# Kernel tuning notes

Measured on AMD Instinct MI355X. Metric: run time of the kernel, lower is better.

## Reference

```python
import jax, jax.numpy as jnp
import numpy as np

N, F, D, H, E = 100000, 256, 128, 4, 1000000
C = D // H  # out_channels per head


def setup_inputs() -> dict:
    key = jax.random.key(0)
    ks = jax.random.split(key, 10)
    glorot = lambda k, shp, fan: jax.random.normal(k, shp, jnp.float32) * (2.0 / sum(fan)) ** 0.5
    return {
        "x": jax.random.normal(ks[0], (N, F), jnp.float32),
        "edge_index_0": jax.random.randint(ks[1], (2, E), 0, N, jnp.int32),
        "edge_index_1": jax.random.randint(ks[2], (2, E), 0, N, jnp.int32),
        "W_lin": glorot(ks[3], (F, D), (F, D)),
        "b_lin": jnp.zeros((D,), jnp.float32),
        "attn_l": glorot(ks[4], (2, H, C), (H, C)),
        "attn_r": glorot(ks[5], (2, H, C), (H, C)),
        "alpha_act": jnp.ones((2,), jnp.float32),  # 'sharpening' init 1.0
        "W_conv": glorot(ks[6], (3, F), (F, 3)),
        "b_conv": jnp.zeros((3,), jnp.float32),
    }


def _segment_softmax(a, seg, n):
    # a: [E, H], seg: [E] destination indices
    amax = jax.ops.segment_max(a, seg, num_segments=n)  # [N, H], -inf for empty segs
    ex = jnp.exp(a - amax[seg])
    denom = jax.ops.segment_sum(ex, seg, num_segments=n)
    return ex / denom[seg]


def reference(x, edge_index_0, edge_index_1, W_lin, b_lin, attn_l, attn_r, alpha_act, W_conv, b_conv):
    # get_h_dict: Linear(F -> D) then reshape [N, H, C]
    h = x @ W_lin + b_lin                      # [N, D]
    hh = h.reshape(N, H, C)
    # get_beta_weights: Conv1d(F, 3, kernel_size=1) on x.unsqueeze(-1) == linear per node; softmax over relations
    beta = jax.nn.softmax(x @ W_conv.T + b_conv, axis=1)  # [N, 3]

    # agg_relation_neighbors: per-metapath GAT-style attention + scatter-add
    rel_outs = []
    for m, ei in enumerate((edge_index_0, edge_index_1)):
        al = jnp.sum(hh * attn_l[m], axis=-1)  # [N, H]
        ar = jnp.sum(hh * attn_r[m], axis=-1)  # [N, H]
        dst, src_j = ei[0], ei[1]              # flow target_to_source: aggregate at edge_index[0]
        a = (ar[src_j] + al[dst]) * alpha_act[m]   # message alpha_j + alpha_i, sharpening activation
        alpha = _segment_softmax(a, dst, N)        # softmax per destination node
        msg = hh[src_j] * alpha[:, :, None]        # [E, H, C]
        rel_outs.append(jax.ops.segment_sum(msg, dst, num_segments=N).reshape(N, D))
    # last relation slot holds the node's own h (first=True)
    emb = jnp.stack(rel_outs + [h], axis=1)        # [N, 3, D]
    out = jnp.einsum('nrd,nr->nd', emb, beta)      # matmul(emb^T, beta).squeeze(-1)
    return jax.nn.relu(out)                        # embedding_activation 'relu'
```

## Files before the change

kernel.cpp:

```cpp
#include <hip/hip_runtime.h>
#include <hip/hip_bf16.h>

#define NN 100000
#define FF 256
#define DD 128
#define EE 1000000
#define NPX (NN / 8)
#define PART_BLOCKS 1024
#define PART_CHUNK ((2 * EE) / (PART_BLOCKS / 8))

typedef __attribute__((ext_vector_type(4))) float f32x4;
typedef __attribute__((ext_vector_type(8))) short bf16x8;

__device__ __forceinline__ ushort f2bf(float f) {
    __hip_bfloat16 h = __float2bfloat16(f);
    return *reinterpret_cast<ushort*>(&h);
}
__device__ __forceinline__ float bf2f(ushort u) {
    return __uint_as_float(((uint)u) << 16);
}

__global__ void pack_w(const float* __restrict__ Wl, ushort* __restrict__ Wt) {
    int id = blockIdx.x * 256 + threadIdx.x;
    int k = id >> 7, n = id & 127;
    Wt[n * FF + k] = f2bf(Wl[id]);
}

__global__ __launch_bounds__(256) void fused_h(const float* __restrict__ x,
                                               const ushort* __restrict__ Wt,
                                               const float* __restrict__ bl,
                                               const float* __restrict__ Wc,
                                               const float* __restrict__ bc,
                                               ushort* __restrict__ hb,
                                               float* __restrict__ beta) {
    __shared__ ushort xs[64][72];
    __shared__ ushort wsT[128][72];
    __shared__ ushort hs[64][136];
    __shared__ float wcs[768];

    int t = threadIdx.x;
    int wv = t >> 6, lane = t & 63;
    int row0 = blockIdx.x * 64;
    int br = t >> 2, bq = t & 3;
    bool rowok = (row0 + br) < NN;

    if (t < 192) ((float4*)wcs)[t] = ((const float4*)Wc)[t];
    __syncthreads();

    f32x4 acc[8];
    #pragma unroll
    for (int i = 0; i < 8; ++i) acc[i] = (f32x4){0.f, 0.f, 0.f, 0.f};

    float bs0 = 0.f, bs1 = 0.f, bs2 = 0.f;

    for (int k0 = 0; k0 < FF; k0 += 64) {
        if (rowok) {
            const float4* xp = (const float4*)(x + (size_t)(row0 + br) * FF + k0 + bq * 16);
            #pragma unroll
            for (int j = 0; j < 4; ++j) {
                float4 v = xp[j];
                int kk = bq * 16 + j * 4;
                const float* w0 = wcs + k0 + kk;
                bs0 += v.x * w0[0] + v.y * w0[1] + v.z * w0[2] + v.w * w0[3];
                const float* w1 = wcs + 256 + k0 + kk;
                bs1 += v.x * w1[0] + v.y * w1[1] + v.z * w1[2] + v.w * w1[3];
                const float* w2 = wcs + 512 + k0 + kk;
                bs2 += v.x * w2[0] + v.y * w2[1] + v.z * w2[2] + v.w * w2[3];
                ushort4 p;
                p.x = f2bf(v.x); p.y = f2bf(v.y); p.z = f2bf(v.z); p.w = f2bf(v.w);
                *(ushort4*)&xs[br][kk] = p;
            }
        } else {
            ushort4 z = {0, 0, 0, 0};
            #pragma unroll
            for (int j = 0; j < 4; ++j) *(ushort4*)&xs[br][bq * 16 + j * 4] = z;
        }
        #pragma unroll
        for (int j = 0; j < 4; ++j) {
            int c = t + 256 * j;
            int rw = c >> 3, seg = c & 7;
            uint4 v = *(const uint4*)(Wt + rw * FF + k0 + seg * 8);
            *(uint4*)&wsT[rw][seg * 8] = v;
        }
        __syncthreads();
        #pragma unroll
        for (int ks = 0; ks < 2; ++ks) {
            bf16x8 af = *(const bf16x8*)&xs[wv * 16 + (lane & 15)][ks * 32 + (lane >> 4) * 8];
            #pragma unroll
            for (int nt = 0; nt < 8; ++nt) {
                bf16x8 bv = *(const bf16x8*)&wsT[nt * 16 + (lane & 15)][ks * 32 + (lane >> 4) * 8];
                acc[nt] = __builtin_amdgcn_mfma_f32_16x16x32_bf16(af, bv, acc[nt], 0, 0, 0);
            }
        }
        __syncthreads();
    }

    bs0 += __shfl_xor(bs0, 1); bs0 += __shfl_xor(bs0, 2);
    bs1 += __shfl_xor(bs1, 1); bs1 += __shfl_xor(bs1, 2);
    bs2 += __shfl_xor(bs2, 1); bs2 += __shfl_xor(bs2, 2);
    if (bq == 0 && rowok) {
        float s0 = bs0 + bc[0], s1 = bs1 + bc[1], s2 = bs2 + bc[2];
        float mx = fmaxf(s0, fmaxf(s1, s2));
        float e0 = __expf(s0 - mx), e1 = __expf(s1 - mx), e2 = __expf(s2 - mx);
        float inv = 1.f / (e0 + e1 + e2);
        int n = row0 + br;
        beta[n * 3 + 0] = e0 * inv;
        beta[n * 3 + 1] = e1 * inv;
        beta[n * 3 + 2] = e2 * inv;
    }

    #pragma unroll
    for (int nt = 0; nt < 8; ++nt) {
        int col = nt * 16 + (lane & 15);
        float bias = bl[col];
        int rbase = wv * 16 + (lane >> 4) * 4;
        #pragma unroll
        for (int r = 0; r < 4; ++r) {
            hs[rbase + r][col] = f2bf(acc[nt][r] + bias);
        }
    }
    __syncthreads();
    #pragma unroll
    for (int j = 0; j < 4; ++j) {
        int c = t + 256 * j;
        int rw = c >> 4, seg = c & 15;
        if (row0 + rw < NN) {
            uint4 v = *(const uint4*)&hs[rw][seg * 8];
            *(uint4*)(hb + (size_t)(row0 + rw) * DD + seg * 8) = v;
        }
    }
}

__global__ __launch_bounds__(256) void alr_kernel(const ushort* __restrict__ hb,
                                                  const float* __restrict__ attn_l,
                                                  const float* __restrict__ attn_r,
                                                  float* __restrict__ AL,
                                                  float* __restrict__ AR) {
    int wid = threadIdx.x >> 6, lane = threadIdx.x & 63;
    int n = blockIdx.x * 4 + wid;
    uint hv = ((const uint*)hb)[(size_t)n * 64 + lane];
    float hx = bf2f((ushort)(hv & 0xffff)), hy = bf2f((ushort)(hv >> 16));
    int hd = lane >> 4;
    int cg = lane & 15;
    #pragma unroll
    for (int m = 0; m < 2; ++m) {
        float2 wl = ((const float2*)attn_l)[m * 64 + hd * 16 + cg];
        float2 wr = ((const float2*)attn_r)[m * 64 + hd * 16 + cg];
        float sl = hx * wl.x + hy * wl.y;
        float sr = hx * wr.x + hy * wr.y;
        for (int off = 1; off < 16; off <<= 1) {
            sl += __shfl_xor(sl, off);
            sr += __shfl_xor(sr, off);
        }
        if (cg == 0) {
            AL[(size_t)(m * NN + n) * 4 + hd] = sl;
            AR[(size_t)(m * NN + n) * 4 + hd] = sr;
        }
    }
}

__global__ __launch_bounds__(256) void count_kernel(const int* __restrict__ ei0,
                                                    const int* __restrict__ ei1,
                                                    int* __restrict__ deg) {
    int b = blockIdx.x;
    int lo = (b & 7) * NPX, hi = lo + NPX;
    int e0 = (b >> 3) * PART_CHUNK;
    for (int i = threadIdx.x; i < PART_CHUNK; i += 256) {
        int e = e0 + i;
        int dst, base;
        if (e < EE) { dst = ei0[e]; base = 0; }
        else        { dst = ei1[e - EE]; base = NN; }
        if (dst >= lo && dst < hi) atomicAdd(&deg[base + dst], 1);
    }
}

__global__ __launch_bounds__(256) void scatter_kernel(const int* __restrict__ ei0,
                                                      const int* __restrict__ ei1,
                                                      const int* __restrict__ rp,
                                                      int* __restrict__ cursor,
                                                      int* __restrict__ srcs) {
    int b = blockIdx.x;
    int lo = (b & 7) * NPX, hi = lo + NPX;
    int e0 = (b >> 3) * PART_CHUNK;
    for (int i = threadIdx.x; i < PART_CHUNK; i += 256) {
        int e = e0 + i;
        int dst, src, base;
        if (e < EE) { dst = ei0[e]; src = ei0[EE + e]; base = 0; }
        else        { int ee = e - EE; dst = ei1[ee]; src = ei1[EE + ee]; base = NN; }
        if (dst >= lo && dst < hi) {
            int idx = base + dst;
            int pos = rp[idx] + atomicAdd(&cursor[idx], 1);
            srcs[pos] = src;
        }
    }
}

__global__ __launch_bounds__(256) void scan1(const int* __restrict__ deg, int* __restrict__ rp,
                                             int* __restrict__ bsum, int L) {
    __shared__ int sm[256];
    int t = threadIdx.x;
    int i = blockIdx.x * 256 + t;
    int v = (i < L) ? deg[i] : 0;
    sm[t] = v;
    __syncthreads();
    for (int off = 1; off < 256; off <<= 1) {
        int o = (t >= off) ? sm[t - off] : 0;
        __syncthreads();
        sm[t] += o;
        __syncthreads();
    }
    if (i < L) rp[i] = sm[t] - v;
    if (t == 255) bsum[blockIdx.x] = sm[255];
}

__global__ __launch_bounds__(256) void scan2(int* __restrict__ bsum, int nb) {
    __shared__ int sm[256];
    int t = threadIdx.x;
    int carry = 0;
    for (int base = 0; base < nb; base += 256) {
        int i = base + t;
        int v = (i < nb) ? bsum[i] : 0;
        __syncthreads();
        sm[t] = v;
        __syncthreads();
        for (int off = 1; off < 256; off <<= 1) {
            int o = (t >= off) ? sm[t - off] : 0;
            __syncthreads();
            sm[t] += o;
            __syncthreads();
        }
        int incl = sm[t];
        int tot = sm[255];
        if (i < nb) bsum[i] = carry + incl - v;
        carry += tot;
    }
}

__global__ void scan3(int* __restrict__ rp, const int* __restrict__ bsum, int L) {
    int i = blockIdx.x * 256 + threadIdx.x;
    if (i < L) rp[i] += bsum[blockIdx.x];
    if (i == 0) rp[L] = 2 * EE;
}

__global__ __launch_bounds__(256) void main_kernel(const ushort* __restrict__ hb,
                                                   const float* __restrict__ AL,
                                                   const float* __restrict__ AR,
                                                   const float* __restrict__ beta,
                                                   const float* __restrict__ alpha_act,
                                                   const int* __restrict__ rp,
                                                   const int* __restrict__ srcs,
                                                   float* __restrict__ out) {
    __shared__ float2 contribs[2][64];
    int w = threadIdx.x >> 6, lane = threadIdx.x & 63;
    int slot = w >> 1, m = w & 1;
    int n = blockIdx.x * 2 + slot;
    const uint* h2 = (const uint*)hb;
    int hd = lane >> 4;

    float alv = AL[(size_t)(m * NN + n) * 4 + hd];
    float am = alpha_act[m];
    float bm = beta[n * 3 + m];
    int e0 = rp[m * NN + n];
    int e1 = rp[m * NN + n + 1];
    const float* ARm = AR + (size_t)m * NN * 4;

    float denom = 0.f, ax = 0.f, ay = 0.f;
    for (int e = e0; e < e1; e += 4) {
        int last = e1 - 1;
        int i1 = min(e + 1, last), i2 = min(e + 2, last), i3 = min(e + 3, last);
        int s0 = srcs[e], s1 = srcs[i1], s2 = srcs[i2], s3 = srcs[i3];
        float r0 = ARm[s0 * 4 + hd];
        float r1 = ARm[s1 * 4 + hd];
        float r2 = ARm[s2 * 4 + hd];
        float r3 = ARm[s3 * 4 + hd];
        uint g0 = h2[(size_t)s0 * 64 + lane];
        uint g1 = h2[(size_t)s1 * 64 + lane];
        uint g2 = h2[(size_t)s2 * 64 + lane];
        uint g3 = h2[(size_t)s3 * 64 + lane];
        float v1 = (e + 1 < e1) ? 1.f : 0.f;
        float v2 = (e + 2 < e1) ? 1.f : 0.f;
        float v3 = (e + 3 < e1) ? 1.f : 0.f;
        float p0 = __expf((r0 + alv) * am);
        float p1 = v1 * __expf((r1 + alv) * am);
        float p2 = v2 * __expf((r2 + alv) * am);
        float p3 = v3 * __expf((r3 + alv) * am);
        denom += (p0 + p1) + (p2 + p3);
        ax += p0 * bf2f((ushort)(g0 & 0xffff)) + p1 * bf2f((ushort)(g1 & 0xffff))
            + p2 * bf2f((ushort)(g2 & 0xffff)) + p3 * bf2f((ushort)(g3 & 0xffff));
        ay += p0 * bf2f((ushort)(g0 >> 16)) + p1 * bf2f((ushort)(g1 >> 16))
            + p2 * bf2f((ushort)(g2 >> 16)) + p3 * bf2f((ushort)(g3 >> 16));
    }
    float invd = (denom > 0.f) ? (1.f / denom) : 0.f;
    float cx = bm * ax * invd;
    float cy = bm * ay * invd;

    if (m == 1) contribs[slot][lane] = make_float2(cx, cy);
    __syncthreads();
    if (m == 0) {
        uint hv = h2[(size_t)n * 64 + lane];
        float b2 = beta[n * 3 + 2];
        float2 c1 = contribs[slot][lane];
        float ox = b2 * bf2f((ushort)(hv & 0xffff)) + cx + c1.x;
        float oy = b2 * bf2f((ushort)(hv >> 16)) + cy + c1.y;
        float2 res;
        res.x = fmaxf(ox, 0.f);
        res.y = fmaxf(oy, 0.f);
        ((float2*)out)[(size_t)n * 64 + lane] = res;
    }
}

extern "C" void kernel_launch(void* const* d_in, const int* in_sizes, int n_in,
                              void* d_out, int out_size, void* d_ws, size_t ws_size,
                              hipStream_t stream) {
    const float* x      = (const float*)d_in[0];
    const int*   ei0    = (const int*)d_in[1];
    const int*   ei1    = (const int*)d_in[2];
    const float* W_lin  = (const float*)d_in[3];
    const float* b_lin  = (const float*)d_in[4];
    const float* attn_l = (const float*)d_in[5];
    const float* attn_r = (const float*)d_in[6];
    const float* alpha  = (const float*)d_in[7];
    const float* W_conv = (const float*)d_in[8];
    const float* b_conv = (const float*)d_in[9];
    float* out = (float*)d_out;

    char* ws = (char*)d_ws;
    size_t off = 0;
    ushort* hb   = (ushort*)(ws + off); off += (size_t)NN * DD * 2;
    ushort* Wt   = (ushort*)(ws + off); off += (size_t)DD * FF * 2;
    float* AL    = (float*)(ws + off);  off += (size_t)2 * NN * 4 * 4;
    float* AR    = (float*)(ws + off);  off += (size_t)2 * NN * 4 * 4;
    float* beta  = (float*)(ws + off);  off += (size_t)NN * 3 * 4;
    int*   deg   = (int*)(ws + off);    off += (size_t)2 * NN * 4;
    int*   cursor= (int*)(ws + off);    off += (size_t)2 * NN * 4;
    int*   rp    = (int*)(ws + off);    off += ((size_t)2 * NN + 4) * 4;
    int*   bsum  = (int*)(ws + off);    off += 1024 * 4;
    int*   srcs  = (int*)(ws + off);    off += (size_t)2 * EE * 4;

    hipMemsetAsync(deg, 0, (size_t)4 * NN * 4, stream);

    pack_w<<<DD * FF / 256, 256, 0, stream>>>(W_lin, Wt);
    fused_h<<<(NN + 63) / 64, 256, 0, stream>>>(x, Wt, b_lin, W_conv, b_conv, hb, beta);
    alr_kernel<<<NN / 4, 256, 0, stream>>>(hb, attn_l, attn_r, AL, AR);
    count_kernel<<<PART_BLOCKS, 256, 0, stream>>>(ei0, ei1, deg);
    int L = 2 * NN;
    int nb = (L + 255) / 256;
    scan1<<<nb, 256, 0, stream>>>(deg, rp, bsum, L);
    scan2<<<1, 256, 0, stream>>>(bsum, nb);
    scan3<<<nb, 256, 0, stream>>>(rp, bsum, L);
    scatter_kernel<<<PART_BLOCKS, 256, 0, stream>>>(ei0, ei1, rp, cursor, srcs);
    main_kernel<<<NN / 2, 256, 0, stream>>>(hb, AL, AR, beta, alpha, rp, srcs, out);
}
```

Baseline: 354.8 us.

## Vectorize edge partition loads and split wave into two edge halves in main kernel

The count and scatter kernels now split work per relation into fixed 8192-edge chunks and read the edge index with int4 loads, with more blocks launched. The main kernel has each half-wave handle alternate edges, with each lane loading 4 bf16 features (uint2) and using 32-bit offset arithmetic. The two halves' partial sums are combined with shuffles, aiming for more gathers in flight per node. The remainder check (e+4<=EE) holds because EE is divisible by 4, and half the lanes sit idle in the epilogue.

```diff
diff --git a/kernel.cpp b/kernel.cpp
--- a/kernel.cpp
+++ b/kernel.cpp
@@ -6,8 +6,8 @@
 #define DD 128
 #define EE 1000000
 #define NPX (NN / 8)
-#define PART_BLOCKS 1024
-#define PART_CHUNK ((2 * EE) / (PART_BLOCKS / 8))
+#define CH 8192
+#define NCH 123
 
 typedef __attribute__((ext_vector_type(4))) float f32x4;
 typedef __attribute__((ext_vector_type(8))) short bf16x8;
@@ -164,13 +164,20 @@
                                                     int* __restrict__ deg) {
     int b = blockIdx.x;
     int lo = (b & 7) * NPX, hi = lo + NPX;
-    int e0 = (b >> 3) * PART_CHUNK;
-    for (int i = threadIdx.x; i < PART_CHUNK; i += 256) {
-        int e = e0 + i;
-        int dst, base;
-        if (e < EE) { dst = ei0[e]; base = 0; }
-        else        { dst = ei1[e - EE]; base = NN; }
-        if (dst >= lo && dst < hi) atomicAdd(&deg[base + dst], 1);
+    int q = b >> 3;
+    int rel = q / NCH, ch = q - rel * NCH;
+    const int* dstrow = rel ? ei1 : ei0;
+    int base = rel * NN;
+    int e0 = ch * CH;
+    for (int i = threadIdx.x; i < CH / 4; i += 256) {
+        int e = e0 + i * 4;
+        if (e + 4 <= EE) {
+            int4 d = *(const int4*)(dstrow + e);
+            if (d.x >= lo && d.x < hi) atomicAdd(&deg[base + d.x], 1);
+            if (d.y >= lo && d.y < hi) atomicAdd(&deg[base + d.y], 1);
+            if (d.z >= lo && d.z < hi) atomicAdd(&deg[base + d.z], 1);
+            if (d.w >= lo && d.w < hi) atomicAdd(&deg[base + d.w], 1);
+        }
     }
 }
 
@@ -181,16 +188,20 @@
                                                       int* __restrict__ srcs) {
     int b = blockIdx.x;
     int lo = (b & 7) * NPX, hi = lo + NPX;
-    int e0 = (b >> 3) * PART_CHUNK;
-    for (int i = threadIdx.x; i < PART_CHUNK; i += 256) {
-        int e = e0 + i;
-        int dst, src, base;
-        if (e < EE) { dst = ei0[e]; src = ei0[EE + e]; base = 0; }
-        else        { int ee = e - EE; dst = ei1[ee]; src = ei1[EE + ee]; base = NN; }
-        if (dst >= lo && dst < hi) {
-            int idx = base + dst;
-            int pos = rp[idx] + atomicAdd(&cursor[idx], 1);
-            srcs[pos] = src;
+    int q = b >> 3;
+    int rel = q / NCH, ch = q - rel * NCH;
+    const int* row = rel ? ei1 : ei0;
+    int base = rel * NN;
+    int e0 = ch * CH;
+    for (int i = threadIdx.x; i < CH / 4; i += 256) {
+        int e = e0 + i * 4;
+        if (e + 4 <= EE) {
+            int4 d = *(const int4*)(row + e);
+            int4 s = *(const int4*)(row + EE + e);
+            if (d.x >= lo && d.x < hi) { int idx = base + d.x; srcs[rp[idx] + atomicAdd(&cursor[idx], 1)] = s.x; }
+            if (d.y >= lo && d.y < hi) { int idx = base + d.y; srcs[rp[idx] + atomicAdd(&cursor[idx], 1)] = s.y; }
+            if (d.z >= lo && d.z < hi) { int idx = base + d.z; srcs[rp[idx] + atomicAdd(&cursor[idx], 1)] = s.z; }
+            if (d.w >= lo && d.w < hi) { int idx = base + d.w; srcs[rp[idx] + atomicAdd(&cursor[idx], 1)] = s.w; }
         }
     }
 }
@@ -250,62 +261,57 @@
                                                    const int* __restrict__ rp,
                                                    const int* __restrict__ srcs,
                                                    float* __restrict__ out) {
-    __shared__ float2 contribs[2][64];
+    __shared__ float4 contribs[2][32];
     int w = threadIdx.x >> 6, lane = threadIdx.x & 63;
     int slot = w >> 1, m = w & 1;
     int n = blockIdx.x * 2 + slot;
-    const uint* h2 = (const uint*)hb;
-    int hd = lane >> 4;
+    int half = lane >> 5, sl = lane & 31;
+    int hd = sl >> 3;
+    const char* h8 = (const char*)hb;
+    const char* ar8 = (const char*)(AR + (size_t)m * NN * 4);
+    const char* sr8 = (const char*)srcs;
+    uint aoff = (uint)(hd << 2);
+    uint hoff = (uint)(sl << 3);
 
     float alv = AL[(size_t)(m * NN + n) * 4 + hd];
     float am = alpha_act[m];
-    float bm = beta[n * 3 + m];
     int e0 = rp[m * NN + n];
     int e1 = rp[m * NN + n + 1];
-    const float* ARm = AR + (size_t)m * NN * 4;
-
-    float denom = 0.f, ax = 0.f, ay = 0.f;
-    for (int e = e0; e < e1; e += 4) {
-        int last = e1 - 1;
-        int i1 = min(e + 1, last), i2 = min(e + 2, last), i3 = min(e + 3, last);
-        int s0 = srcs[e], s1 = srcs[i1], s2 = srcs[i2], s3 = srcs[i3];
-        float r0 = ARm[s0 * 4 + hd];
-        float r1 = ARm[s1 * 4 + hd];
-        float r2 = ARm[s2 * 4 + hd];
-        float r3 = ARm[s3 * 4 + hd];
-        uint g0 = h2[(size_t)s0 * 64 + lane];
-        uint g1 = h2[(size_t)s1 * 64 + lane];
-        uint g2 = h2[(size_t)s2 * 64 + lane];
-        uint g3 = h2[(size_t)s3 * 64 + lane];
-        float v1 = (e + 1 < e1) ? 1.f : 0.f;
-        float v2 = (e + 2 < e1) ? 1.f : 0.f;
-        float v3 = (e + 3 < e1) ? 1.f : 0.f;
-        float p0 = __expf((r0 + alv) * am);
-        float p1 = v1 * __expf((r1 + alv) * am);
-        float p2 = v2 * __expf((r2 + alv) * am);
-        float p3 = v3 * __expf((r3 + alv) * am);
-        denom += (p0 + p1) + (p2 + p3);
-        ax += p0 * bf2f((ushort)(g0 & 0xffff)) + p1 * bf2f((ushort)(g1 & 0xffff))
-            + p2 * bf2f((ushort)(g2 & 0xffff)) + p3 * bf2f((ushort)(g3 & 0xffff));
-        ay += p0 * bf2f((ushort)(g0 >> 16)) + p1 * bf2f((ushort)(g1 >> 16))
-            + p2 * bf2f((ushort)(g2 >> 16)) + p3 * bf2f((ushort)(g3 >> 16));
-    }
+
+    float denom = 0.f, a0 = 0.f, a1 = 0.f, a2 = 0.f, a3 = 0.f;
+    for (int k = e0 + half; k < e1; k += 2) {
+        int s = *(const int*)(sr8 + ((uint)k << 2));
+        float r = *(const float*)(ar8 + ((uint)s * 16u + aoff));
+        uint2 g = *(const uint2*)(h8 + ((uint)s * 256u + hoff));
+        float p = __expf((r + alv) * am);
+        denom += p;
+        a0 = fmaf(p, __uint_as_float(g.x << 16), a0);
+        a1 = fmaf(p, __uint_as_float(g.x & 0xffff0000u), a1);
+        a2 = fmaf(p, __uint_as_float(g.y << 16), a2);
+        a3 = fmaf(p, __uint_as_float(g.y & 0xffff0000u), a3);
+    }
+    denom += __shfl_xor(denom, 32);
+    a0 += __shfl_xor(a0, 32);
+    a1 += __shfl_xor(a1, 32);
+    a2 += __shfl_xor(a2, 32);
+    a3 += __shfl_xor(a3, 32);
     float invd = (denom > 0.f) ? (1.f / denom) : 0.f;
-    float cx = bm * ax * invd;
-    float cy = bm * ay * invd;
-
-    if (m == 1) contribs[slot][lane] = make_float2(cx, cy);
+    float bm = beta[n * 3 + m] * invd;
+    float4 c;
+    c.x = a0 * bm; c.y = a1 * bm; c.z = a2 * bm; c.w = a3 * bm;
+
+    if (m == 1 && half == 0) contribs[slot][sl] = c;
     __syncthreads();
-    if (m == 0) {
-        uint hv = h2[(size_t)n * 64 + lane];
+    if (m == 0 && half == 0) {
+        uint2 hv = *(const uint2*)(h8 + ((uint)n * 256u + hoff));
         float b2 = beta[n * 3 + 2];
-        float2 c1 = contribs[slot][lane];
-        float ox = b2 * bf2f((ushort)(hv & 0xffff)) + cx + c1.x;
-        float oy = b2 * bf2f((ushort)(hv >> 16)) + cy + c1.y;
-        float2 res;
-        res.x = fmaxf(ox, 0.f);
-        res.y = fmaxf(oy, 0.f);
-        ((float2*)out)[(size_t)n * 64 + lane] = res;
+        float4 c1 = contribs[slot][sl];
+        float4 res;
+        res.x = fmaxf(fmaf(b2, __uint_as_float(hv.x << 16), c.x + c1.x), 0.f);
+        res.y = fmaxf(fmaf(b2, __uint_as_float(hv.x & 0xffff0000u), c.y + c1.y), 0.f);
+        res.z = fmaxf(fmaf(b2, __uint_as_float(hv.y << 16), c.z + c1.z), 0.f);
+        res.w = fmaxf(fmaf(b2, __uint_as_float(hv.y & 0xffff0000u), c.w + c1.w), 0.f);
+        *(float4*)(out + (size_t)n * 128 + sl * 4) = res;
     }
 }
 
@@ -342,12 +348,12 @@
     pack_w<<<DD * FF / 256, 256, 0, stream>>>(W_lin, Wt);
     fused_h<<<(NN + 63) / 64, 256, 0, stream>>>(x, Wt, b_lin, W_conv, b_conv, hb, beta);
     alr_kernel<<<NN / 4, 256, 0, stream>>>(hb, attn_l, attn_r, AL, AR);
-    count_kernel<<<PART_BLOCKS, 256, 0, stream>>>(ei0, ei1, deg);
+    count_kernel<<<2 * 8 * NCH, 256, 0, stream>>>(ei0, ei1, deg);
     int L = 2 * NN;
     int nb = (L + 255) / 256;
     scan1<<<nb, 256, 0, stream>>>(deg, rp, bsum, L);
     scan2<<<1, 256, 0, stream>>>(bsum, nb);
     scan3<<<nb, 256, 0, stream>>>(rp, bsum, L);
-    scatter_kernel<<<PART_BLOCKS, 256, 0, stream>>>(ei0, ei1, rp, cursor, srcs);
+    scatter_kernel<<<2 * 8 * NCH, 256, 0, stream>>>(ei0, ei1, rp, cursor, srcs);
     main_kernel<<<NN / 2, 256, 0, stream>>>(hb, AL, AR, beta, alpha, rp, srcs, out);
 }
```

Measured after the change: 398.2 us. 12.2% more time.
